# Kernel optimization log

Measured on AMD Instinct MI355X. Metric: run time of the kernel, lower is better.

The kernel has to match this reference:

```python
import jax, jax.numpy as jnp
import numpy as np

BATCH, SEQ, D_MODEL = 2, 4096, 1024
D_STATE, EXPAND = 64, 2
D_INNER = D_MODEL * EXPAND


def setup_inputs() -> dict:
    key = jax.random.key(0)
    ks = jax.random.split(key, 12)
    s = 0.02
    return {
        "x": jax.random.normal(ks[0], (BATCH, SEQ, D_MODEL), dtype=jnp.float32),
        "W_in": jax.random.normal(ks[1], (D_MODEL, 2 * D_INNER), dtype=jnp.float32) * s,
        "b_in": jnp.zeros((2 * D_INNER,), dtype=jnp.float32),
        "W_xp": jax.random.normal(ks[2], (D_INNER, D_STATE), dtype=jnp.float32) * s,
        "b_xp": jnp.zeros((D_STATE,), dtype=jnp.float32),
        "W_dt": jax.random.normal(ks[3], (D_INNER, D_MODEL), dtype=jnp.float32) * s,
        "b_dt": jnp.zeros((D_MODEL,), dtype=jnp.float32),
        "W_out": jax.random.normal(ks[4], (D_INNER, D_MODEL), dtype=jnp.float32) * s,
        "b_out": jnp.zeros((D_MODEL,), dtype=jnp.float32),
        "A_log": jax.random.normal(ks[5], (D_STATE,), dtype=jnp.float32),
        "D": jax.random.normal(ks[6], (D_MODEL,), dtype=jnp.float32),
    }


def _silu(v):
    return v * jax.nn.sigmoid(v)


def reference(x, W_in, b_in, W_xp, b_xp, W_dt, b_dt, W_out, b_out, A_log, D):
    # in_proj -> split into inner stream and residual gate
    xr = x @ W_in + b_in                       # [B,S,2*d_inner]
    x_inner, res = jnp.split(xr, 2, axis=-1)   # each [B,S,d_inner]
    x_inner = _silu(x_inner)

    A = -jnp.exp(A_log)                        # [N]
    delta = jax.nn.softplus(x_inner @ W_dt + b_dt)  # [B,S,d_model]
    mean_delta = delta.mean(axis=-1)           # [B,S] (scalar dt per step, as in source)
    a = jnp.exp(A[None, None, :] * mean_delta[..., None])  # [B,S,N] discrete A
    bx = x_inner @ W_xp + b_xp                 # [B,S,N] input injection

    # sequential selective-scan recurrence: state = a_t * state + bx_t
    def step(state, inp):
        a_t, bx_t = inp                        # [B,N] each
        state = a_t * state + bx_t
        return state, state.sum(axis=-1)       # emit per-batch scalar

    init = jnp.zeros((x.shape[0], D_STATE), dtype=x.dtype)
    _, s_sum = jax.lax.scan(step, init, (a.transpose(1, 0, 2), bx.transpose(1, 0, 2)))
    s_sum = s_sum.T                            # [B,S]

    y = s_sum[..., None] * x_inner             # [B,S,d_inner]
    y = y * _silu(res)
    out = y @ W_out + b_out + x * D
    return out
```

## Files before the change

### kernel.cpp

```cpp
#include <hip/hip_runtime.h>

#define SEQ 4096
#define DMODEL 1024
#define DSTATE 64
#define DINNER 2048
#define MROWS 8192
#define NCAT 1152
#define NCHUNK 64
#define LCHUNK 64

typedef __attribute__((ext_vector_type(8))) __bf16 bf16x8;
typedef __attribute__((ext_vector_type(8))) short short8;
typedef __attribute__((ext_vector_type(4))) float floatx4;

__device__ inline float bf2f(short s) {
  union { unsigned u; float f; } c;
  c.u = ((unsigned)(unsigned short)s) << 16;
  return c.f;
}
__device__ inline short f2bf(float f) {
  union { float f; unsigned u; } c; c.f = f;
  unsigned r = 0x7fffu + ((c.u >> 16) & 1u);
  return (short)((c.u + r) >> 16);
}
__device__ inline float silu_f(float v) {
  return v * __builtin_amdgcn_rcpf(1.f + __expf(-v));
}
__device__ inline float softplus_f(float v) {
  return fmaxf(v, 0.f) + log1pf(__expf(-fabsf(v)));
}
__device__ inline void gld_lds16(const void* g, void* l) {
  __builtin_amdgcn_global_load_lds(
      (__attribute__((address_space(1))) void*)g,
      (__attribute__((address_space(3))) void*)l, 16, 0, 0);
}

__device__ inline size_t permOff(int r, int k, int K) {
  return (((size_t)(r >> 4) * (K >> 3) + (k >> 3)) << 7) + ((r & 15) << 3) + (k & 7);
}

#define PP0 4096
#define PP1 (PP0 + 4096)
#define PP2 (PP1 + 2048)
#define PP3 (PP2 + 128)
#define PP4 (PP3 + 2048)

__device__ void tile_transpose_perm(const float* __restrict__ in, short* __restrict__ out,
                                    int R, int C, int bx, int by, float (*tile)[33]) {
  const int tx = threadIdx.x & 31, ty = threadIdx.x >> 5;
  const int cb = bx * 32, rb = by * 32;
#pragma unroll
  for (int i = 0; i < 32; i += 8) {
    int r = rb + ty + i, c = cb + tx;
    tile[ty + i][tx] = (r < R && c < C) ? in[(size_t)r * C + c] : 0.f;
  }
  __syncthreads();
#pragma unroll
  for (int i = 0; i < 32; i += 8) {
    int orow = cb + ty + i, oc = rb + tx;
    if (orow < C && oc < R) out[permOff(orow, oc, R)] = f2bf(tile[tx][ty + i]);
  }
}

__global__ void prepass_kernel(const float* __restrict__ x, short* __restrict__ x_bf,
                               const float* __restrict__ W_in, short* __restrict__ Wt_in,
                               const float* __restrict__ W_dt, const float* __restrict__ W_xp,
                               short* __restrict__ Bcat,
                               const float* __restrict__ W_out, short* __restrict__ Wt_out) {
  __shared__ float tile[32][33];
  const int blk = blockIdx.x;
  if (blk < PP0) {
    int o = blk * 256 + threadIdx.x;
    int m = o & 15, rest = o >> 4;
    int c = rest & 127, p = rest >> 7;
    const float* src = x + ((size_t)(p * 16 + m)) * 1024 + c * 8;
    float4 v0 = ((const float4*)src)[0];
    float4 v1 = ((const float4*)src)[1];
    short8 ov;
    ov[0] = f2bf(v0.x); ov[1] = f2bf(v0.y); ov[2] = f2bf(v0.z); ov[3] = f2bf(v0.w);
    ov[4] = f2bf(v1.x); ov[5] = f2bf(v1.y); ov[6] = f2bf(v1.z); ov[7] = f2bf(v1.w);
    ((short8*)x_bf)[o] = ov;
  } else if (blk < PP1) {
    int t = blk - PP0;
    tile_transpose_perm(W_in, Wt_in, 1024, 4096, t & 127, t >> 7, tile);
  } else if (blk < PP2) {
    int t = blk - PP1;
    tile_transpose_perm(W_dt, Bcat, 2048, 1024, t & 31, t >> 5, tile);
  } else if (blk < PP3) {
    int t = blk - PP2;
    tile_transpose_perm(W_xp, Bcat + (size_t)1024 * DINNER, 2048, 64, t & 1, t >> 1, tile);
  } else {
    int t = blk - PP3;
    tile_transpose_perm(W_out, Wt_out, 2048, 1024, t & 31, t >> 5, tile);
  }
}

template <int MODE, int KTOT, int KSL, int NB, int Z>
__global__ __launch_bounds__(256) void gemm_bt(
    const short* __restrict__ A, const short* __restrict__ Bt,
    const float* __restrict__ bias,
    void* __restrict__ out0, void* __restrict__ out1)
{
  __shared__ __attribute__((aligned(16))) short sA[128 * 64];
  __shared__ __attribute__((aligned(16))) short sB[128 * 64];

  const int tid = threadIdx.x;
  const int lane = tid & 63;
  const int w = tid >> 6;
  const int wr = w >> 1, wc = w & 1;
  const int m = lane & 15, quad = lane >> 4;

  const int xcd = blockIdx.x & 7;
  const int rest = blockIdx.x >> 3;
  constexpr int PXB = 8 * NB;
  const int z = rest / PXB;
  const int q2 = rest - z * PXB;
  const int bM = (xcd * 8 + (q2 & 7)) * 128;
  const int bN = (q2 >> 3) * 128;
  constexpr int N = NB * 128;

  floatx4 acc[4][4] = {};

  const size_t PS = (size_t)KTOT * 16;
  const short* Apan0 = A  + ((size_t)(bM >> 4) + w) * PS + lane * 8;
  const short* Apan1 = Apan0 + 4 * PS;
  const short* Bpan0 = Bt + ((size_t)(bN >> 4) + w) * PS + lane * 8;
  const short* Bpan1 = Bpan0 + 4 * PS;
  short* dA0 = sA + w * 1024;
  short* dA1 = sA + (w + 4) * 1024;
  short* dB0 = sB + w * 1024;
  short* dB1 = sB + (w + 4) * 1024;

  const int kbeg = z * KSL;
  for (int k0 = kbeg; k0 < kbeg + KSL; k0 += 64) {
    __syncthreads();
    const size_t ko = (size_t)k0 * 16;
    gld_lds16(Apan0 + ko,       dA0);
    gld_lds16(Apan0 + ko + 512, dA0 + 512);
    gld_lds16(Apan1 + ko,       dA1);
    gld_lds16(Apan1 + ko + 512, dA1 + 512);
    gld_lds16(Bpan0 + ko,       dB0);
    gld_lds16(Bpan0 + ko + 512, dB0 + 512);
    gld_lds16(Bpan1 + ko,       dB1);
    gld_lds16(Bpan1 + ko + 512, dB1 + 512);
    __syncthreads();
#pragma unroll
    for (int kh = 0; kh < 2; ++kh) {
      bf16x8 af[4], bf[4];
#pragma unroll
      for (int rt = 0; rt < 4; ++rt)
        af[rt] = *(const bf16x8*)(sA + (wr * 4 + rt) * 1024 + (kh * 4 + quad) * 128 + m * 8);
#pragma unroll
      for (int ct = 0; ct < 4; ++ct)
        bf[ct] = *(const bf16x8*)(sB + (wc * 4 + ct) * 1024 + (kh * 4 + quad) * 128 + m * 8);
#pragma unroll
      for (int rt = 0; rt < 4; ++rt)
#pragma unroll
        for (int ct = 0; ct < 4; ++ct)
          acc[rt][ct] = __builtin_amdgcn_mfma_f32_16x16x32_bf16(af[rt], bf[ct], acc[rt][ct], 0, 0, 0);
    }
  }

  const int rowbase = bM + wr * 64;
  const int colbase = bN + wc * 64;

  if (MODE == 0) {
    short* dst = (bN < DINNER) ? (short*)out0 : (short*)out1;
    const int cb = (bN < DINNER) ? colbase : colbase - DINNER;
#pragma unroll
    for (int rt = 0; rt < 4; ++rt) {
      const size_t rowPan = ((size_t)((rowbase >> 4) + rt)) << 8;
#pragma unroll
      for (int ct = 0; ct < 4; ++ct) {
        const int colA = colbase + ct * 16 + m;
        const int colP = cb + ct * 16 + m;
        const size_t base = ((rowPan + (colP >> 3)) << 7) + (colP & 7) + ((size_t)quad * 32);
#pragma unroll
        for (int reg = 0; reg < 4; ++reg) {
          float val = acc[rt][ct][reg] + bias[colA];
          dst[base + reg * 8] = f2bf(silu_f(val));
        }
      }
    }
  } else {
    if (NB == 9 && colbase >= 1088) return;
    short* dst = (short*)out0 + (size_t)z * MROWS * N;
#pragma unroll
    for (int rt = 0; rt < 4; ++rt)
#pragma unroll
      for (int ct = 0; ct < 4; ++ct) {
        const int col = colbase + ct * 16 + m;
#pragma unroll
        for (int reg = 0; reg < 4; ++reg) {
          const int r = rowbase + rt * 16 + quad * 4 + reg;
          dst[(size_t)r * N + col] = f2bf(acc[rt][ct][reg]);
        }
      }
  }
}

__global__ void g2_epilogue(const short* __restrict__ p, const float* __restrict__ b_dt,
                            const float* __restrict__ b_xp,
                            float* __restrict__ md_sum, float* __restrict__ bx) {
  const int row = blockIdx.x * 4 + (threadIdx.x >> 6);
  const int lane = threadIdx.x & 63;
  const size_t base0 = (size_t)row * NCAT;
  const size_t base1 = base0 + (size_t)MROWS * NCAT;
  short8 a0 = *(const short8*)(p + base0 + lane * 16);
  short8 a1 = *(const short8*)(p + base0 + lane * 16 + 8);
  short8 c0 = *(const short8*)(p + base1 + lane * 16);
  short8 c1 = *(const short8*)(p + base1 + lane * 16 + 8);
  float s = 0.f;
#pragma unroll
  for (int j = 0; j < 8; ++j) {
    s += softplus_f(bf2f(a0[j]) + bf2f(c0[j]) + b_dt[lane * 16 + j]);
    s += softplus_f(bf2f(a1[j]) + bf2f(c1[j]) + b_dt[lane * 16 + 8 + j]);
  }
  s += __shfl_xor(s, 1);  s += __shfl_xor(s, 2);  s += __shfl_xor(s, 4);
  s += __shfl_xor(s, 8);  s += __shfl_xor(s, 16); s += __shfl_xor(s, 32);
  if (lane == 0) md_sum[row] = s;
  bx[(size_t)row * DSTATE + lane] =
      bf2f(p[base0 + 1024 + lane]) + bf2f(p[base1 + 1024 + lane]) + b_xp[lane];
}

__global__ void g4_epilogue(const short* __restrict__ p, const float* __restrict__ b_out,
                            const float* __restrict__ x, const float* __restrict__ Dv,
                            float* __restrict__ out) {
  const int r = blockIdx.x, c = threadIdx.x * 4;
  const size_t o = (size_t)r * DMODEL + c;
  short4 a0 = *(const short4*)(p + o);
  short4 a1 = *(const short4*)(p + (size_t)MROWS * DMODEL + o);
  float4 xv = *(const float4*)(x + o);
  float4 ov;
  ov.x = bf2f(a0.x) + bf2f(a1.x) + b_out[c + 0] + xv.x * Dv[c + 0];
  ov.y = bf2f(a0.y) + bf2f(a1.y) + b_out[c + 1] + xv.y * Dv[c + 1];
  ov.z = bf2f(a0.z) + bf2f(a1.z) + b_out[c + 2] + xv.z * Dv[c + 2];
  ov.w = bf2f(a0.w) + bf2f(a1.w) + b_out[c + 3] + xv.w * Dv[c + 3];
  *(float4*)(out + o) = ov;
}

__global__ void scan_phase1(const float* __restrict__ md_sum, const float* __restrict__ A_log,
                            const float* __restrict__ bx,
                            float* __restrict__ chunk_prod, float* __restrict__ chunk_end) {
  const int n = threadIdx.x;
  const int c = blockIdx.x & (NCHUNK - 1);
  const int b = blockIdx.x >> 6;
  const float An = -__expf(A_log[n]);
  float prod = 1.f, st = 0.f;
  const int t0 = c * LCHUNK;
#pragma unroll 4
  for (int i = 0; i < LCHUNK; ++i) {
    const int t = t0 + i;
    const float md = md_sum[b * SEQ + t] * (1.f / DMODEL);
    const float a = __expf(An * md);
    st = a * st + bx[((size_t)(b * SEQ + t)) * DSTATE + n];
    prod *= a;
  }
  chunk_prod[(b * NCHUNK + c) * DSTATE + n] = prod;
  chunk_end [(b * NCHUNK + c) * DSTATE + n] = st;
}

__global__ void scan_phase3(const float* __restrict__ md_sum, const float* __restrict__ A_log,
                            const float* __restrict__ bx,
                            const float* __restrict__ chunk_prod,
                            const float* __restrict__ chunk_end,
                            float* __restrict__ s_sum) {
  const int n = threadIdx.x;
  const int c = blockIdx.x & (NCHUNK - 1);
  const int b = blockIdx.x >> 6;
  const float An = -__expf(A_log[n]);
  float st = 0.f;
  for (int cc = 0; cc < c; ++cc) {
    const size_t idx = ((size_t)(b * NCHUNK + cc)) * DSTATE + n;
    st = chunk_prod[idx] * st + chunk_end[idx];
  }
  const int t0 = c * LCHUNK;
#pragma unroll 4
  for (int i = 0; i < LCHUNK; ++i) {
    const int t = t0 + i;
    const float md = md_sum[b * SEQ + t] * (1.f / DMODEL);
    const float a = __expf(An * md);
    st = a * st + bx[((size_t)(b * SEQ + t)) * DSTATE + n];
    float v = st;
    v += __shfl_xor(v, 32); v += __shfl_xor(v, 16); v += __shfl_xor(v, 8);
    v += __shfl_xor(v, 4);  v += __shfl_xor(v, 2);  v += __shfl_xor(v, 1);
    if (n == 0) s_sum[b * SEQ + t] = v;
  }
}

__global__ void ymul_kernel(const short* __restrict__ xi, const short* __restrict__ g,
                            const float* __restrict__ s_sum, short* __restrict__ y) {
  const int o = blockIdx.x * 256 + threadIdx.x;
  const int row = ((o >> 12) << 4) | (o & 15);
  const size_t base = (size_t)o * 8;
  const float s = s_sum[row];
  short8 xv = *(const short8*)(xi + base);
  short8 gv = *(const short8*)(g + base);
  short8 yv;
#pragma unroll
  for (int k = 0; k < 8; ++k) yv[k] = f2bf(s * bf2f(xv[k]) * bf2f(gv[k]));
  *(short8*)(y + base) = yv;
}

extern "C" void kernel_launch(void* const* d_in, const int* in_sizes, int n_in,
                              void* d_out, int out_size, void* d_ws, size_t ws_size,
                              hipStream_t stream) {
  const float* x     = (const float*)d_in[0];
  const float* W_in  = (const float*)d_in[1];
  const float* b_in  = (const float*)d_in[2];
  const float* W_xp  = (const float*)d_in[3];
  const float* b_xp  = (const float*)d_in[4];
  const float* W_dt  = (const float*)d_in[5];
  const float* b_dt  = (const float*)d_in[6];
  const float* W_out = (const float*)d_in[7];
  const float* b_out = (const float*)d_in[8];
  const float* A_log = (const float*)d_in[9];
  const float* Dv    = (const float*)d_in[10];

  char* ws = (char*)d_ws;
  size_t off = 0;
  auto alloc = [&](size_t bytes) -> void* {
    void* p = (void*)(ws + off);
    off += (bytes + 255) & ~(size_t)255;
    return p;
  };
  short* x_bf    = (short*)alloc((size_t)MROWS * DMODEL * 2);
  short* Wt_in   = (short*)alloc((size_t)4096 * 1024 * 2);
  short* Bcat    = (short*)alloc((size_t)NCAT * DINNER * 2);
  short* Wt_out  = (short*)alloc((size_t)1024 * 2048 * 2);
  short* xi      = (short*)alloc((size_t)MROWS * DINNER * 2);
  short* gbuf    = (short*)alloc((size_t)MROWS * DINNER * 2);
  short* ybuf    = (short*)alloc((size_t)MROWS * DINNER * 2);
  short* p2      = (short*)alloc((size_t)2 * MROWS * NCAT * 2);
  float* md_sum  = (float*)alloc((size_t)MROWS * 4);
  float* bx      = (float*)alloc((size_t)MROWS * DSTATE * 4);
  float* cprod   = (float*)alloc((size_t)2 * NCHUNK * DSTATE * 4);
  float* cend    = (float*)alloc((size_t)2 * NCHUNK * DSTATE * 4);
  float* s_sum   = (float*)alloc((size_t)MROWS * 4);

  prepass_kernel<<<PP4, 256, 0, stream>>>(x, x_bf, W_in, Wt_in, W_dt, W_xp, Bcat, W_out, Wt_out);

  gemm_bt<0, 1024, 1024, 32, 1><<<2048, 256, 0, stream>>>(x_bf, Wt_in, b_in, xi, gbuf);
  gemm_bt<1, 2048, 1024, 9, 2><<<1152, 256, 0, stream>>>(xi, Bcat, nullptr, p2, nullptr);
  g2_epilogue<<<MROWS / 4, 256, 0, stream>>>(p2, b_dt, b_xp, md_sum, bx);
  scan_phase1<<<2 * NCHUNK, DSTATE, 0, stream>>>(md_sum, A_log, bx, cprod, cend);
  scan_phase3<<<2 * NCHUNK, DSTATE, 0, stream>>>(md_sum, A_log, bx, cprod, cend, s_sum);
  ymul_kernel<<<MROWS * DINNER / 8 / 256, 256, 0, stream>>>(xi, gbuf, s_sum, ybuf);
  gemm_bt<1, 2048, 1024, 8, 2><<<1024, 256, 0, stream>>>(ybuf, Wt_out, nullptr, xi, nullptr);
  g4_epilogue<<<MROWS, 256, 0, stream>>>(xi, b_out, x, Dv, (float*)d_out);
}
```

Measured before the change: 417.2 us.

## Add 256x256-tile 512-thread GEMM with 4-stage LDS pipeline for in/out projections

Introduces a new GEMM kernel that computes 256x256 output tiles with 8 waves per block, each wave holding an 8x4 grid of MFMA accumulators. K-tiles are staged through a four-slot LDS ring via direct global-to-LDS loads, with three tiles kept in flight. The kernel replaces the smaller-tile GEMM for the input projection and the output projection, aiming for more operand reuse per LDS byte and fewer global loads. In exchange, register pressure is higher, fewer blocks are launched (512 and 256), and the LDS footprint grows to 128 KB per block, which may reduce occupancy and tail efficiency.

After: 423.1 us. No clear change (+1.4%).

```diff
diff --git a/kernel.cpp b/kernel.cpp
--- a/kernel.cpp
+++ b/kernel.cpp
@@ -199,6 +199,122 @@
   }
 }
 
+template <int MODE, int KTOT, int KSL, int NT, int ZS>
+__global__ __launch_bounds__(512, 2) void gemm256(
+    const short* __restrict__ A, const short* __restrict__ Bt,
+    const float* __restrict__ bias,
+    void* __restrict__ out0, void* __restrict__ out1)
+{
+  __shared__ __attribute__((aligned(16))) short sA[4 * 8192];
+  __shared__ __attribute__((aligned(16))) short sB[4 * 8192];
+
+  const int tid = threadIdx.x;
+  const int lane = tid & 63;
+  const int w = tid >> 6;
+  const int wr = w >> 2, wc = w & 3;
+  const int m = lane & 15, quad = lane >> 4;
+
+  const int xcd = blockIdx.x & 7;
+  const int q = blockIdx.x >> 3;
+  const int mt = xcd * 4 + (q & 3);
+  const int rest = q >> 2;
+  const int ntile = rest % NT;
+  const int z = rest / NT;
+  const int bM = mt * 256, bN = ntile * 256;
+  const int kbeg = z * KSL;
+
+  floatx4 acc[8][4] = {};
+
+  const size_t PS = (size_t)KTOT * 16;
+  const short* Ag0 = A  + ((size_t)(bM >> 4) + w) * PS + (size_t)kbeg * 16 + lane * 8;
+  const short* Ag1 = Ag0 + 8 * PS;
+  const short* Bg0 = Bt + ((size_t)(bN >> 4) + w) * PS + (size_t)kbeg * 16 + lane * 8;
+  const short* Bg1 = Bg0 + 8 * PS;
+
+  constexpr int NTILES = KSL / 32;
+
+  auto STAGE = [&](int t, int slot) {
+    const size_t go = (size_t)t << 9;
+    short* da = sA + slot * 8192 + w * 512;
+    short* db = sB + slot * 8192 + w * 512;
+    gld_lds16(Ag0 + go, da);
+    gld_lds16(Ag1 + go, da + 4096);
+    gld_lds16(Bg0 + go, db);
+    gld_lds16(Bg1 + go, db + 4096);
+  };
+  auto COMPUTE = [&](int slot) {
+    const short* sa = sA + slot * 8192 + wr * 4096 + quad * 128 + m * 8;
+    const short* sb = sB + slot * 8192 + wc * 2048 + quad * 128 + m * 8;
+    bf16x8 af[8], bf[4];
+#pragma unroll
+    for (int rt = 0; rt < 8; ++rt) af[rt] = *(const bf16x8*)(sa + rt * 512);
+#pragma unroll
+    for (int ct = 0; ct < 4; ++ct) bf[ct] = *(const bf16x8*)(sb + ct * 512);
+#pragma unroll
+    for (int rt = 0; rt < 8; ++rt)
+#pragma unroll
+      for (int ct = 0; ct < 4; ++ct)
+        acc[rt][ct] = __builtin_amdgcn_mfma_f32_16x16x32_bf16(af[rt], bf[ct], acc[rt][ct], 0, 0, 0);
+  };
+
+  STAGE(0, 0); STAGE(1, 1); STAGE(2, 2);
+  asm volatile("s_waitcnt vmcnt(8)" ::: "memory");
+  __builtin_amdgcn_s_barrier();
+
+#pragma unroll 1
+  for (int t = 0; t < NTILES - 3; ++t) {
+    STAGE(t + 3, (t + 3) & 3);
+    COMPUTE(t & 3);
+    asm volatile("s_waitcnt vmcnt(8)" ::: "memory");
+    __builtin_amdgcn_s_barrier();
+  }
+  COMPUTE((NTILES - 3) & 3);
+  asm volatile("s_waitcnt vmcnt(4)" ::: "memory");
+  __builtin_amdgcn_s_barrier();
+  COMPUTE((NTILES - 2) & 3);
+  asm volatile("s_waitcnt vmcnt(0)" ::: "memory");
+  __builtin_amdgcn_s_barrier();
+  COMPUTE((NTILES - 1) & 3);
+
+  const int rowbase = bM + wr * 128;
+  const int colbase = bN + wc * 64;
+
+  if constexpr (MODE == 0) {
+    short* dst = (bN < DINNER) ? (short*)out0 : (short*)out1;
+    const int cb = (bN < DINNER) ? colbase : colbase - DINNER;
+#pragma unroll
+    for (int rt = 0; rt < 8; ++rt) {
+      const size_t rowPan = ((size_t)(rowbase >> 4) + rt) << 8;
+#pragma unroll
+      for (int ct = 0; ct < 4; ++ct) {
+        const int colA = colbase + ct * 16 + m;
+        const int colP = cb + ct * 16 + m;
+        const size_t base = ((rowPan + (colP >> 3)) << 7) + (colP & 7) + ((size_t)quad * 32);
+        const float bv = bias[colA];
+#pragma unroll
+        for (int reg = 0; reg < 4; ++reg) {
+          float val = acc[rt][ct][reg] + bv;
+          dst[base + reg * 8] = f2bf(silu_f(val));
+        }
+      }
+    }
+  } else {
+    constexpr int N = NT * 256;
+    short* dst = (short*)out0 + (size_t)z * MROWS * N;
+#pragma unroll
+    for (int rt = 0; rt < 8; ++rt)
+#pragma unroll
+      for (int ct = 0; ct < 4; ++ct) {
+        const int col = colbase + ct * 16 + m;
+#pragma unroll
+        for (int reg = 0; reg < 4; ++reg) {
+          const int r = rowbase + rt * 16 + quad * 4 + reg;
+          dst[(size_t)r * N + col] = f2bf(acc[rt][ct][reg]);
+        }
+      }
+  }
+}
+
 __global__ void g2_epilogue(const short* __restrict__ p, const float* __restrict__ b_dt,
                             const float* __restrict__ b_xp,
                             float* __restrict__ md_sum, float* __restrict__ bx) {
@@ -340,12 +456,12 @@
 
   prepass_kernel<<<PP4, 256, 0, stream>>>(x, x_bf, W_in, Wt_in, W_dt, W_xp, Bcat, W_out, Wt_out);
 
-  gemm_bt<0, 1024, 1024, 32, 1><<<2048, 256, 0, stream>>>(x_bf, Wt_in, b_in, xi, gbuf);
+  gemm256<0, 1024, 1024, 16, 1><<<512, 512, 0, stream>>>(x_bf, Wt_in, b_in, xi, gbuf);
   gemm_bt<1, 2048, 1024, 9, 2><<<1152, 256, 0, stream>>>(xi, Bcat, nullptr, p2, nullptr);
   g2_epilogue<<<MROWS / 4, 256, 0, stream>>>(p2, b_dt, b_xp, md_sum, bx);
   scan_phase1<<<2 * NCHUNK, DSTATE, 0, stream>>>(md_sum, A_log, bx, cprod, cend);
   scan_phase3<<<2 * NCHUNK, DSTATE, 0, stream>>>(md_sum, A_log, bx, cprod, cend, s_sum);
   ymul_kernel<<<MROWS * DINNER / 8 / 256, 256, 0, stream>>>(xi, gbuf, s_sum, ybuf);
-  gemm_bt<1, 2048, 1024, 8, 2><<<1024, 256, 0, stream>>>(ybuf, Wt_out, nullptr, xi, nullptr);
+  gemm256<1, 2048, 1024, 4, 2><<<256, 512, 0, stream>>>(ybuf, Wt_out, nullptr, xi, nullptr);
   g4_epilogue<<<MROWS, 256, 0, stream>>>(xi, b_out, x, Dv, (float*)d_out);
 }
```
